# Performance work log

Measured on AMD Instinct MI355X. Metric: run time of the kernel, lower is better.

Reference implementation:

```python
import jax, jax.numpy as jnp
import numpy as np

N_STRIDE = 128  # 'n' from __init__: stride between subsequences


def make_mask(S, m, n):
    # Faithful vectorization of create_mask: overlap of windows [i*n, i*n+m).
    # overlap_ratio = max(0, m - |i-j|*n) / m; mask True iff (0.5 <= ratio < 1) or i == j.
    # (ratio >= 1 only happens at i == j, which the first branch already catches.)
    idx = jnp.arange(S)
    diff = jnp.abs(idx[:, None] - idx[None, :])
    ratio = jnp.maximum(0, m - diff * n).astype(jnp.float32) / m
    return ((ratio >= 0.5) & (ratio < 1.0)) | (diff == 0)


def setup_inputs() -> dict:
    key = jax.random.key(0)
    k1, k2, k3 = jax.random.split(key, 3)
    B, D, S, L = 8, 8, 512, 256  # batch, num_dims, num_subsequences, seq_length(=d_model)
    x = jax.random.normal(k1, (B, D, S, L), jnp.float32)
    qkv_w = jax.random.normal(k2, (3 * L, L), jnp.float32) * (1.0 / np.sqrt(L))
    qkv_b = jax.random.normal(k3, (3 * L,), jnp.float32) * 0.02
    return {"x": x, "qkv_w": qkv_w, "qkv_b": qkv_b}


def reference(x, qkv_w, qkv_b):
    B, D, S, L = x.shape
    # Batched over the per-channel Python loop in the original.
    qkv = jnp.einsum('bdsl,ol->bdso', x, qkv_w) + qkv_b  # [B,D,S,3L]
    q, k, v = jnp.split(qkv, 3, axis=-1)
    attn = jnp.einsum('bdsh,bdth->bdst', q, k) / jnp.sqrt(jnp.float32(L))
    attn = jax.nn.softmax(attn, axis=-1)
    mask = make_mask(S, L, N_STRIDE)  # m = d_model = L
    attn = jnp.where(mask, jnp.float32(0), attn)  # masked_fill(mask, 0)
    out = jnp.einsum('bdst,bdth->bdsh', attn, v).reshape(B, D * S, L)
    # Block-diagonal scatter of per-channel attention maps: [B, D*S, D*S]
    z = jnp.zeros((B, D, S, D, S), attn.dtype)
    z = z.at[:, jnp.arange(D), :, jnp.arange(D), :].set(jnp.transpose(attn, (1, 0, 2, 3)))
    block = z.reshape(B, D * S, D * S)
    return out, block
```

## Files before the change

kernel.cpp:

```cpp
#include <hip/hip_runtime.h>

typedef unsigned short u16;
typedef __attribute__((ext_vector_type(8))) short bf16x8;
typedef __attribute__((ext_vector_type(4))) float f32x4;

#define NS 512
#define NL 256
#define NBD 64
#define OUT_ELEMS 8388608u

__device__ __forceinline__ u16 f2bf(float f) {
  union { float f; unsigned u; } v; v.f = f;
  unsigned u = v.u;
  unsigned r = (u + 0x7FFFu + ((u >> 16) & 1u)) >> 16;
  return (u16)r;
}

__device__ __forceinline__ bf16x8 pack8(float4 a, float4 b) {
  bf16x8 r;
  r[0] = (short)f2bf(a.x); r[1] = (short)f2bf(a.y);
  r[2] = (short)f2bf(a.z); r[3] = (short)f2bf(a.w);
  r[4] = (short)f2bf(b.x); r[5] = (short)f2bf(b.y);
  r[6] = (short)f2bf(b.z); r[7] = (short)f2bf(b.w);
  return r;
}

__device__ __forceinline__ bf16x8 pack8v(f32x4 a, f32x4 b) {
  bf16x8 r;
  r[0] = (short)f2bf(a[0]); r[1] = (short)f2bf(a[1]);
  r[2] = (short)f2bf(a[2]); r[3] = (short)f2bf(a[3]);
  r[4] = (short)f2bf(b[0]); r[5] = (short)f2bf(b[1]);
  r[6] = (short)f2bf(b[2]); r[7] = (short)f2bf(b[3]);
  return r;
}

__global__ __launch_bounds__(256) void qkv_kernel(
    const float* __restrict__ x, const float* __restrict__ w,
    const float* __restrict__ bias,
    u16* __restrict__ qws, u16* __restrict__ kws, u16* __restrict__ vws)
{
  __shared__ u16 wlds[64][264];

  const int t = threadIdx.x;
  const int wave = t >> 6, lane = t & 63;
  const int r16 = lane & 15, kg = lane >> 4;
  const int row0 = blockIdx.x * 64;
  const int srow = row0 + wave * 16 + r16;

  bf16x8 a[8];
  {
    const float* xr = x + (size_t)srow * NL;
    for (int ks = 0; ks < 8; ++ks) {
      float4 f0 = *(const float4*)(xr + ks * 32 + kg * 8);
      float4 f1 = *(const float4*)(xr + ks * 32 + kg * 8 + 4);
      a[ks] = pack8(f0, f1);
    }
  }

  const int wr = t >> 2, qq = t & 3;
  for (int ct = 0; ct < 12; ++ct) {
    const int col0 = ct * 64;
    __syncthreads();
    {
      const float* src = w + (size_t)(col0 + wr) * NL + qq * 64;
      u16* dst = &wlds[wr][qq * 64];
      for (int j = 0; j < 64; j += 8) {
        float4 f0 = *(const float4*)(src + j);
        float4 f1 = *(const float4*)(src + j + 4);
        *(bf16x8*)(void*)(dst + j) = pack8(f0, f1);
      }
    }
    __syncthreads();

    for (int cf = 0; cf < 4; ++cf) {
      const int cl = cf * 16 + r16;
      f32x4 acc = {0.f, 0.f, 0.f, 0.f};
      for (int ks = 0; ks < 8; ++ks) {
        bf16x8 b = *(const bf16x8*)(void*)&wlds[cl][ks * 32 + kg * 8];
        acc = __builtin_amdgcn_mfma_f32_16x16x32_bf16(a[ks], b, acc, 0, 0, 0);
      }
      const int o = col0 + cl;
      const float bv = bias[o];
      for (int i = 0; i < 4; ++i) {
        const float val = acc[i] + bv;
        const int grow = row0 + wave * 16 + kg * 4 + i;
        const int bd = grow >> 9, s = grow & 511;
        const u16 h = f2bf(val);
        if (o < 256)      qws[((size_t)bd * NS + s) * NL + o] = h;
        else if (o < 512) kws[((size_t)bd * NS + s) * NL + (o - 256)] = h;
        else              vws[((size_t)bd * NL + (o - 512)) * NS + s] = h;
      }
    }
  }
}

__global__ __launch_bounds__(256) void attn_kernel(
    const u16* __restrict__ qws, const u16* __restrict__ kws,
    const u16* __restrict__ vws, float* __restrict__ out)
{
  __shared__ float Sm[32][516];
  __shared__ float red[32][8];
  __shared__ float rowstat[32];

  const int rt = blockIdx.x, bd = blockIdx.y;
  const int b = bd >> 3, d = bd & 7;
  const int t = threadIdx.x, wave = t >> 6, lane = t & 63;
  const int r16 = lane & 15, kg = lane >> 4;
  const size_t ch = (size_t)bd * NS * NL;

  bf16x8 aq[2][8];
  for (int rf = 0; rf < 2; ++rf) {
    const int s1 = rt * 32 + rf * 16 + r16;
    const u16* p = qws + ch + (size_t)s1 * NL + kg * 8;
    for (int ks = 0; ks < 8; ++ks)
      aq[rf][ks] = *(const bf16x8*)(p + ks * 32);
  }

  for (int cf = 0; cf < 8; ++cf) {
    const int s2 = wave * 128 + cf * 16 + r16;
    const u16* p = kws + ch + (size_t)s2 * NL + kg * 8;
    f32x4 acc0 = {0, 0, 0, 0}, acc1 = {0, 0, 0, 0};
    for (int ks = 0; ks < 8; ++ks) {
      bf16x8 bfr = *(const bf16x8*)(p + ks * 32);
      acc0 = __builtin_amdgcn_mfma_f32_16x16x32_bf16(aq[0][ks], bfr, acc0, 0, 0, 0);
      acc1 = __builtin_amdgcn_mfma_f32_16x16x32_bf16(aq[1][ks], bfr, acc1, 0, 0, 0);
    }
    const int c = wave * 128 + cf * 16 + r16;
    for (int i = 0; i < 4; ++i) {
      Sm[kg * 4 + i][c]      = acc0[i] * 0.0625f;
      Sm[16 + kg * 4 + i][c] = acc1[i] * 0.0625f;
    }
  }
  __syncthreads();

  const int r = t >> 3, c8 = t & 7;
  float m = -1e30f;
  for (int j = 0; j < 8; ++j)
    for (int u = 0; u < 8; ++u)
      m = fmaxf(m, Sm[r][c8 * 8 + j * 64 + u]);
  red[r][c8] = m;
  __syncthreads();
  if (t < 32) {
    float mm = red[t][0];
    for (int j = 1; j < 8; ++j) mm = fmaxf(mm, red[t][j]);
    rowstat[t] = mm;
  }
  __syncthreads();
  const float rm = rowstat[r];
  float ssum = 0.f;
  for (int j = 0; j < 8; ++j)
    for (int u = 0; u < 8; ++u) {
      const int c = c8 * 8 + j * 64 + u;
      const float e = __expf(Sm[r][c] - rm);
      Sm[r][c] = e;
      ssum += e;
    }
  red[r][c8] = ssum;
  __syncthreads();
  if (t < 32) {
    float s = 0.f;
    for (int j = 0; j < 8; ++j) s += red[t][j];
    rowstat[t] = 1.0f / s;
  }
  __syncthreads();

  const float inv = rowstat[r];
  const int s1g = rt * 32 + r;
  float* brow = out + OUT_ELEMS + ((size_t)b << 24) +
                (size_t)(d * NS + s1g) * 4096 + d * NS;
  for (int j = 0; j < 8; ++j) {
    const int cbase = c8 * 8 + j * 64;
    f32x4 v0, v1;
    for (int u = 0; u < 4; ++u) {
      const int c = cbase + u;
      float v = Sm[r][c] * inv;
      const int dd = c > s1g ? c - s1g : s1g - c;
      if (dd <= 1) v = 0.f;
      Sm[r][c] = v;
      v0[u] = v;
    }
    for (int u = 0; u < 4; ++u) {
      const int c = cbase + 4 + u;
      float v = Sm[r][c] * inv;
      const int dd = c > s1g ? c - s1g : s1g - c;
      if (dd <= 1) v = 0.f;
      Sm[r][c] = v;
      v1[u] = v;
    }
    __builtin_nontemporal_store(v0, (f32x4*)(brow + cbase));
    __builtin_nontemporal_store(v1, (f32x4*)(brow + cbase + 4));
  }
  __syncthreads();

  f32x4 accO[2][4];
  for (int rf = 0; rf < 2; ++rf)
    for (int cf = 0; cf < 4; ++cf) accO[rf][cf] = (f32x4){0, 0, 0, 0};
  for (int ks = 0; ks < 16; ++ks) {
    bf16x8 pa[2];
    for (int rf = 0; rf < 2; ++rf) {
      const float* p = &Sm[rf * 16 + r16][ks * 32 + kg * 8];
      pa[rf] = pack8v(*(const f32x4*)p, *(const f32x4*)(p + 4));
    }
    for (int cf = 0; cf < 4; ++cf) {
      const int f = wave * 64 + cf * 16 + r16;
      bf16x8 bv = *(const bf16x8*)(vws + ((size_t)bd * NL + f) * NS + ks * 32 + kg * 8);
      accO[0][cf] = __builtin_amdgcn_mfma_f32_16x16x32_bf16(pa[0], bv, accO[0][cf], 0, 0, 0);
      accO[1][cf] = __builtin_amdgcn_mfma_f32_16x16x32_bf16(pa[1], bv, accO[1][cf], 0, 0, 0);
    }
  }
  for (int rf = 0; rf < 2; ++rf)
    for (int cf = 0; cf < 4; ++cf) {
      const int fcol = wave * 64 + cf * 16 + r16;
      for (int i = 0; i < 4; ++i) {
        const int s1 = rt * 32 + rf * 16 + kg * 4 + i;
        __builtin_nontemporal_store(accO[rf][cf][i],
            out + (size_t)b * (4096u * 256u) + (size_t)(d * NS + s1) * NL + fcol);
      }
    }

  {
    const f32x4 z4 = {0.f, 0.f, 0.f, 0.f};
    float* base = out + OUT_ELEMS + ((size_t)b << 24) +
                  (size_t)(d * NS + rt * 32) * 4096;
    const int dlo = d << 7;
    for (int idx = t; idx < 32 * 1024; idx += 256) {
      const int row = idx >> 10, c4 = idx & 1023;
      if ((unsigned)(c4 - dlo) >= 128u)
        __builtin_nontemporal_store(z4, (f32x4*)(base + (size_t)row * 4096) + c4);
    }
  }
}

extern "C" void kernel_launch(void* const* d_in, const int* in_sizes, int n_in,
                              void* d_out, int out_size, void* d_ws, size_t ws_size,
                              hipStream_t stream) {
  const float* x    = (const float*)d_in[0];
  const float* w    = (const float*)d_in[1];
  const float* bias = (const float*)d_in[2];
  float* out = (float*)d_out;

  u16* qws = (u16*)d_ws;
  u16* kws = qws + (size_t)NBD * NS * NL;
  u16* vws = kws + (size_t)NBD * NS * NL;

  qkv_kernel<<<dim3(512), 256, 0, stream>>>(x, w, bias, qws, kws, vws);
  attn_kernel<<<dim3(16, 64), 256, 0, stream>>>(qws, kws, vws, out);
}
```

Before: 289.2 us.

## Halve attention row tile to 16 rows and use wave-shuffle softmax reductions

```diff
diff --git a/kernel.cpp b/kernel.cpp
--- a/kernel.cpp
+++ b/kernel.cpp
@@ -94,136 +94,111 @@
   }
 }
 
-__global__ __launch_bounds__(256) void attn_kernel(
+__global__ __launch_bounds__(256, 4) void attn_kernel(
     const u16* __restrict__ qws, const u16* __restrict__ kws,
     const u16* __restrict__ vws, float* __restrict__ out)
 {
-  __shared__ float Sm[32][516];
-  __shared__ float red[32][8];
-  __shared__ float rowstat[32];
+  __shared__ float Sm[16][516];
+  __shared__ float rowinv[16];
 
   const int rt = blockIdx.x, bd = blockIdx.y;
   const int b = bd >> 3, d = bd & 7;
   const int t = threadIdx.x, wave = t >> 6, lane = t & 63;
   const int r16 = lane & 15, kg = lane >> 4;
   const size_t ch = (size_t)bd * NS * NL;
-
-  bf16x8 aq[2][8];
-  for (int rf = 0; rf < 2; ++rf) {
-    const int s1 = rt * 32 + rf * 16 + r16;
-    const u16* p = qws + ch + (size_t)s1 * NL + kg * 8;
+  const int row0 = rt * 16;
+
+  bf16x8 aq[8];
+  {
+    const u16* p = qws + ch + (size_t)(row0 + r16) * NL + kg * 8;
     for (int ks = 0; ks < 8; ++ks)
-      aq[rf][ks] = *(const bf16x8*)(p + ks * 32);
+      aq[ks] = *(const bf16x8*)(p + ks * 32);
   }
 
   for (int cf = 0; cf < 8; ++cf) {
     const int s2 = wave * 128 + cf * 16 + r16;
     const u16* p = kws + ch + (size_t)s2 * NL + kg * 8;
-    f32x4 acc0 = {0, 0, 0, 0}, acc1 = {0, 0, 0, 0};
+    f32x4 acc = {0, 0, 0, 0};
     for (int ks = 0; ks < 8; ++ks) {
       bf16x8 bfr = *(const bf16x8*)(p + ks * 32);
-      acc0 = __builtin_amdgcn_mfma_f32_16x16x32_bf16(aq[0][ks], bfr, acc0, 0, 0, 0);
-      acc1 = __builtin_amdgcn_mfma_f32_16x16x32_bf16(aq[1][ks], bfr, acc1, 0, 0, 0);
+      acc = __builtin_amdgcn_mfma_f32_16x16x32_bf16(aq[ks], bfr, acc, 0, 0, 0);
     }
     const int c = wave * 128 + cf * 16 + r16;
-    for (int i = 0; i < 4; ++i) {
-      Sm[kg * 4 + i][c]      = acc0[i] * 0.0625f;
-      Sm[16 + kg * 4 + i][c] = acc1[i] * 0.0625f;
-    }
+    for (int i = 0; i < 4; ++i)
+      Sm[kg * 4 + i][c] = acc[i] * 0.0625f;
   }
   __syncthreads();
 
-  const int r = t >> 3, c8 = t & 7;
-  float m = -1e30f;
-  for (int j = 0; j < 8; ++j)
-    for (int u = 0; u < 8; ++u)
-      m = fmaxf(m, Sm[r][c8 * 8 + j * 64 + u]);
-  red[r][c8] = m;
+  {
+    const int row = wave * 4 + (lane >> 4);
+    const int c16 = lane & 15;
+    float m = -1e30f;
+    for (int j = 0; j < 32; ++j)
+      m = fmaxf(m, Sm[row][c16 + j * 16]);
+    m = fmaxf(m, __shfl_xor(m, 1));
+    m = fmaxf(m, __shfl_xor(m, 2));
+    m = fmaxf(m, __shfl_xor(m, 4));
+    m = fmaxf(m, __shfl_xor(m, 8));
+    float s = 0.f;
+    for (int j = 0; j < 32; ++j) {
+      const int c = c16 + j * 16;
+      const float e = __expf(Sm[row][c] - m);
+      Sm[row][c] = e;
+      s += e;
+    }
+    s += __shfl_xor(s, 1);
+    s += __shfl_xor(s, 2);
+    s += __shfl_xor(s, 4);
+    s += __shfl_xor(s, 8);
+    if (c16 == 0) rowinv[row] = 1.0f / s;
+  }
   __syncthreads();
-  if (t < 32) {
-    float mm = red[t][0];
-    for (int j = 1; j < 8; ++j) mm = fmaxf(mm, red[t][j]);
-    rowstat[t] = mm;
+
+  for (int k = 0; k < 8; ++k) {
+    const int slot = t + k * 256;
+    const int row = slot >> 7, c4 = slot & 127;
+    const float inv = rowinv[row];
+    const int s1g = row0 + row;
+    f32x4 e4 = *(const f32x4*)&Sm[row][c4 * 4];
+    f32x4 p;
+    for (int u = 0; u < 4; ++u) {
+      const int c = c4 * 4 + u;
+      const int dd = c > s1g ? c - s1g : s1g - c;
+      p[u] = (dd <= 1) ? 0.f : e4[u] * inv;
+    }
+    *(f32x4*)&Sm[row][c4 * 4] = p;
+    float* brow = out + OUT_ELEMS + ((size_t)b << 24) +
+                  (size_t)(d * NS + s1g) * 4096 + d * NS;
+    __builtin_nontemporal_store(p, (f32x4*)brow + c4);
   }
   __syncthreads();
-  const float rm = rowstat[r];
-  float ssum = 0.f;
-  for (int j = 0; j < 8; ++j)
-    for (int u = 0; u < 8; ++u) {
-      const int c = c8 * 8 + j * 64 + u;
-      const float e = __expf(Sm[r][c] - rm);
-      Sm[r][c] = e;
-      ssum += e;
-    }
-  red[r][c8] = ssum;
-  __syncthreads();
-  if (t < 32) {
-    float s = 0.f;
-    for (int j = 0; j < 8; ++j) s += red[t][j];
-    rowstat[t] = 1.0f / s;
-  }
-  __syncthreads();
-
-  const float inv = rowstat[r];
-  const int s1g = rt * 32 + r;
-  float* brow = out + OUT_ELEMS + ((size_t)b << 24) +
-                (size_t)(d * NS + s1g) * 4096 + d * NS;
-  for (int j = 0; j < 8; ++j) {
-    const int cbase = c8 * 8 + j * 64;
-    f32x4 v0, v1;
-    for (int u = 0; u < 4; ++u) {
-      const int c = cbase + u;
-      float v = Sm[r][c] * inv;
-      const int dd = c > s1g ? c - s1g : s1g - c;
-      if (dd <= 1) v = 0.f;
-      Sm[r][c] = v;
-      v0[u] = v;
-    }
-    for (int u = 0; u < 4; ++u) {
-      const int c = cbase + 4 + u;
-      float v = Sm[r][c] * inv;
-      const int dd = c > s1g ? c - s1g : s1g - c;
-      if (dd <= 1) v = 0.f;
-      Sm[r][c] = v;
-      v1[u] = v;
-    }
-    __builtin_nontemporal_store(v0, (f32x4*)(brow + cbase));
-    __builtin_nontemporal_store(v1, (f32x4*)(brow + cbase + 4));
-  }
-  __syncthreads();
-
-  f32x4 accO[2][4];
-  for (int rf = 0; rf < 2; ++rf)
-    for (int cf = 0; cf < 4; ++cf) accO[rf][cf] = (f32x4){0, 0, 0, 0};
+
+  f32x4 accO[4];
+  for (int cf = 0; cf < 4; ++cf) accO[cf] = (f32x4){0, 0, 0, 0};
   for (int ks = 0; ks < 16; ++ks) {
-    bf16x8 pa[2];
-    for (int rf = 0; rf < 2; ++rf) {
-      const float* p = &Sm[rf * 16 + r16][ks * 32 + kg * 8];
-      pa[rf] = pack8v(*(const f32x4*)p, *(const f32x4*)(p + 4));
-    }
+    const float* p = &Sm[r16][ks * 32 + kg * 8];
+    bf16x8 pa = pack8v(*(const f32x4*)p, *(const f32x4*)(p + 4));
     for (int cf = 0; cf < 4; ++cf) {
       const int f = wave * 64 + cf * 16 + r16;
       bf16x8 bv = *(const bf16x8*)(vws + ((size_t)bd * NL + f) * NS + ks * 32 + kg * 8);
-      accO[0][cf] = __builtin_amdgcn_mfma_f32_16x16x32_bf16(pa[0], bv, accO[0][cf], 0, 0, 0);
-      accO[1][cf] = __builtin_amdgcn_mfma_f32_16x16x32_bf16(pa[1], bv, accO[1][cf], 0, 0, 0);
-    }
-  }
-  for (int rf = 0; rf < 2; ++rf)
-    for (int cf = 0; cf < 4; ++cf) {
-      const int fcol = wave * 64 + cf * 16 + r16;
-      for (int i = 0; i < 4; ++i) {
-        const int s1 = rt * 32 + rf * 16 + kg * 4 + i;
-        __builtin_nontemporal_store(accO[rf][cf][i],
-            out + (size_t)b * (4096u * 256u) + (size_t)(d * NS + s1) * NL + fcol);
-      }
-    }
+      accO[cf] = __builtin_amdgcn_mfma_f32_16x16x32_bf16(pa, bv, accO[cf], 0, 0, 0);
+    }
+  }
+  for (int cf = 0; cf < 4; ++cf) {
+    const int fcol = wave * 64 + cf * 16 + r16;
+    for (int i = 0; i < 4; ++i) {
+      const int s1 = row0 + kg * 4 + i;
+      __builtin_nontemporal_store(accO[cf][i],
+          out + (size_t)b * (4096u * 256u) + (size_t)(d * NS + s1) * NL + fcol);
+    }
+  }
 
   {
     const f32x4 z4 = {0.f, 0.f, 0.f, 0.f};
     float* base = out + OUT_ELEMS + ((size_t)b << 24) +
-                  (size_t)(d * NS + rt * 32) * 4096;
+                  (size_t)(d * NS + row0) * 4096;
     const int dlo = d << 7;
-    for (int idx = t; idx < 32 * 1024; idx += 256) {
+    for (int idx = t; idx < 16 * 1024; idx += 256) {
       const int row = idx >> 10, c4 = idx & 1023;
       if ((unsigned)(c4 - dlo) >= 128u)
         __builtin_nontemporal_store(z4, (f32x4*)(base + (size_t)row * 4096) + c4);
@@ -244,5 +219,5 @@
   u16* vws = kws + (size_t)NBD * NS * NL;
 
   qkv_kernel<<<dim3(512), 256, 0, stream>>>(x, w, bias, qws, kws, vws);
-  attn_kernel<<<dim3(16, 64), 256, 0, stream>>>(qws, kws, vws, out);
-}
+  attn_kernel<<<dim3(32, 64), 256, 0, stream>>>(qws, kws, vws, out);
+}
```

Result: slower. 297.4 us (+2.8%).
